# Optimization experiments

Measured on AMD Instinct MI355X. Metric: run time of the kernel, lower is better.

## Reference

```python
import jax, jax.numpy as jnp
import numpy as np

N_GENES = 3072
N_CELLS = 3072
HIDDEN = 64
CAUSAL = 16
CS = 32
ALPHA = 0.35  # LeakyReLU negative slope
NEG_BIG = -9.0e15


def setup_inputs() -> dict:
    key = jax.random.key(0)
    ks = jax.random.split(key, 20)
    s = 0.05
    return {
        "x": jax.random.normal(ks[0], (N_CELLS, N_GENES), jnp.float32),
        "adj": jax.random.randint(ks[1], (N_GENES, N_GENES), 0, 2, jnp.int32),
        "eps": jax.random.normal(ks[2], (N_GENES, CAUSAL), jnp.float32),
        "W_gat": jax.random.normal(ks[3], (N_CELLS, HIDDEN), jnp.float32) * s,
        "a_gat": jax.random.normal(ks[4], (2 * HIDDEN,), jnp.float32) * s,
        "W_mu": jax.random.normal(ks[5], (HIDDEN, CAUSAL), jnp.float32) * s,
        "b_mu": jnp.zeros((CAUSAL,), jnp.float32),
        "W_lv": jax.random.normal(ks[6], (HIDDEN, CAUSAL), jnp.float32) * s,
        "b_lv": jnp.zeros((CAUSAL,), jnp.float32),
        "W_diff": jax.random.normal(ks[7], (CAUSAL + HIDDEN, CS), jnp.float32) * s,
        "b_diff": jnp.zeros((CS,), jnp.float32),
        "W_dec": jax.random.normal(ks[8], (CS, N_CELLS), jnp.float32) * s,
        "b_dec": jnp.zeros((N_CELLS,), jnp.float32),
        "W_gcn1": jax.random.normal(ks[9], (N_CELLS, HIDDEN), jnp.float32) * s,
        "W_gcn2": jax.random.normal(ks[10], (HIDDEN, HIDDEN), jnp.float32) * s,
    }


def _gcn(xg, adjf, W):
    # adj + I, symmetric normalization D^-1/2 A D^-1/2, then A_norm @ (x @ W), relu
    A = adjf + jnp.eye(adjf.shape[0], dtype=adjf.dtype)
    d = A.sum(axis=1)
    d_inv_sqrt = jnp.where(d > 0, d ** -0.5, 0.0)
    A_norm = d_inv_sqrt[:, None] * A * d_inv_sqrt[None, :]
    return jax.nn.relu(A_norm @ (xg @ W))


def reference(x, adj, eps, W_gat, a_gat, W_mu, b_mu, W_lv, b_lv,
              W_diff, b_diff, W_dec, b_dec, W_gcn1, W_gcn2):
    adjf = adj.astype(jnp.float32)
    # ---- GAT layer (batch of 1, squeezed). h: (M, F)
    h = x.T @ W_gat
    F = h.shape[1]
    # a_input[i, j] = concat(h_j, h_i)  => e_ij = leakyrelu(a1.h_j + a2.h_i)
    s_dst = h @ a_gat[:F]   # contribution of column index j
    s_src = h @ a_gat[F:]   # contribution of row index i
    e = jax.nn.leaky_relu(s_src[:, None] + s_dst[None, :], ALPHA)
    e = jnp.where(adjf > 0, e, NEG_BIG)
    att = jax.nn.softmax(e, axis=1)  # dropout p=0.1 is identity in eval mode
    h_gat = jax.nn.elu(att @ h)      # (M, HIDDEN)
    # ---- causal VAE encode + reparameterize
    mu = h_gat @ W_mu + b_mu
    logvar = h_gat @ W_lv + b_lv
    z = mu + eps * jnp.exp(0.5 * logvar)
    # ---- diffusion fusion
    cs = jax.nn.relu(jnp.concatenate([z, h_gat], axis=-1) @ W_diff + b_diff)
    # ---- decoder
    x_recon = jax.nn.sigmoid(cs @ W_dec + b_dec)  # (M, N_CELLS)
    # ---- inference model (two GCN layers on x_recon.T, as in original code)
    h1 = _gcn(x_recon.T, adjf, W_gcn1)
    h2 = _gcn(h1, adjf, W_gcn2)
    ie = jnp.concatenate([h2, cs], axis=-1)
    return (x_recon, h2, ie, cs, mu, logvar)
```

## Files before the change

kernel.cpp:

```cpp
#include <hip/hip_runtime.h>
#include <math.h>

#define N 3072
#define H 64
#define CAUS 16
#define CSD 32
#define GAT_ALPHA 0.35f
#define SLICES 16
#define JSL (N / SLICES)
#define NH (N * H)
typedef unsigned long long u64;
typedef unsigned short u16;
typedef __attribute__((ext_vector_type(4))) float f32x4;
typedef __attribute__((ext_vector_type(8))) short s16x8;
struct alignas(8) u16x4 { u16 x, y, z, w; };
struct T4 { float4 r[4]; };

__device__ inline u16 f2bf(float f) {
  unsigned u = __builtin_bit_cast(unsigned, f);
  u += 0x7fffu + ((u >> 16) & 1u);
  return (u16)(u >> 16);
}

__device__ inline T4 t_load(const float* __restrict__ src, int ld, int t) {
  int k4 = (t >> 4) * 4, m4 = (t & 15) * 4;
  T4 o;
#pragma unroll
  for (int d = 0; d < 4; d++)
    o.r[d] = *(const float4*)(src + (size_t)(k4 + d) * ld + m4);
  return o;
}
__device__ inline void t_store(u16 (&dst)[64][72], const T4& v, int t) {
  int k4 = (t >> 4) * 4, m4 = (t & 15) * 4;
  u16x4 c0 = {f2bf(v.r[0].x), f2bf(v.r[1].x), f2bf(v.r[2].x), f2bf(v.r[3].x)};
  u16x4 c1 = {f2bf(v.r[0].y), f2bf(v.r[1].y), f2bf(v.r[2].y), f2bf(v.r[3].y)};
  u16x4 c2 = {f2bf(v.r[0].z), f2bf(v.r[1].z), f2bf(v.r[2].z), f2bf(v.r[3].z)};
  u16x4 c3 = {f2bf(v.r[0].w), f2bf(v.r[1].w), f2bf(v.r[2].w), f2bf(v.r[3].w)};
  *(u16x4*)&dst[m4 + 0][k4] = c0;
  *(u16x4*)&dst[m4 + 1][k4] = c1;
  *(u16x4*)&dst[m4 + 2][k4] = c2;
  *(u16x4*)&dst[m4 + 3][k4] = c3;
}

__global__ __launch_bounds__(256) void k_pack(const int* __restrict__ adj,
                                              u64* __restrict__ packed,
                                              float* __restrict__ dis) {
  int row = blockIdx.x * 4 + (threadIdx.x >> 6);
  int lane = threadIdx.x & 63;
  const int* ar = adj + (size_t)row * N;
  int deg = 0;
  for (int w = 0; w < 48; w++) {
    int v = ar[w * 64 + lane];
    u64 m = __ballot(v > 0);
    if (lane == 0) packed[(size_t)row * 48 + w] = m;
    deg += (v > 0) ? 1 : 0;
  }
  for (int off = 32; off; off >>= 1) deg += __shfl_xor(deg, off);
  if (lane == 0) dis[row] = rsqrtf((float)deg + 1.0f);
}

__global__ __launch_bounds__(256) void k_mm32(const float* __restrict__ A, int lda,
                                              const float* __restrict__ B, int ldb,
                                              float* __restrict__ outp) {
  __shared__ u16 As[32][72];
  __shared__ u16 Bs[64][72];
  int t = threadIdx.x;
  int g0 = blockIdx.x * 32;
  int c0 = blockIdx.y * JSL;
  int w = t >> 6, l = t & 63, il = l & 15, kg = l >> 4;
  int ri = w & 1, cj = w >> 1;
  int ak = (t >> 3) * 2, am = (t & 7) * 4;
  f32x4 acc0 = {0.f, 0.f, 0.f, 0.f}, acc1 = {0.f, 0.f, 0.f, 0.f};
  float4 a0 = *(const float4*)(A + (size_t)(c0 + ak) * lda + g0 + am);
  float4 a1 = *(const float4*)(A + (size_t)(c0 + ak + 1) * lda + g0 + am);
  T4 bv = t_load(B + (size_t)c0 * ldb, ldb, t);
  for (int cb = 0; cb < JSL; cb += 64) {
    __syncthreads();
    As[am + 0][ak] = f2bf(a0.x); As[am + 1][ak] = f2bf(a0.y);
    As[am + 2][ak] = f2bf(a0.z); As[am + 3][ak] = f2bf(a0.w);
    As[am + 0][ak + 1] = f2bf(a1.x); As[am + 1][ak + 1] = f2bf(a1.y);
    As[am + 2][ak + 1] = f2bf(a1.z); As[am + 3][ak + 1] = f2bf(a1.w);
    t_store(Bs, bv, t);
    if (cb + 64 < JSL) {
      a0 = *(const float4*)(A + (size_t)(c0 + cb + 64 + ak) * lda + g0 + am);
      a1 = *(const float4*)(A + (size_t)(c0 + cb + 65 + ak) * lda + g0 + am);
      bv = t_load(B + (size_t)(c0 + cb + 64) * ldb, ldb, t);
    }
    __syncthreads();
#pragma unroll
    for (int kk = 0; kk < 64; kk += 32) {
      s16x8 a = *(const s16x8*)&As[ri * 16 + il][kk + kg * 8];
      s16x8 b0 = *(const s16x8*)&Bs[cj * 32 + il][kk + kg * 8];
      s16x8 b1 = *(const s16x8*)&Bs[cj * 32 + 16 + il][kk + kg * 8];
      acc0 = __builtin_amdgcn_mfma_f32_16x16x32_bf16(a, b0, acc0, 0, 0, 0);
      acc1 = __builtin_amdgcn_mfma_f32_16x16x32_bf16(a, b1, acc1, 0, 0, 0);
    }
  }
  float* ob = outp + (size_t)blockIdx.y * NH;
#pragma unroll
  for (int c = 0; c < 2; c++) {
    f32x4 acc = c ? acc1 : acc0;
    int col = cj * 32 + c * 16 + il;
    int rbase = g0 + ri * 16 + kg * 4;
#pragma unroll
    for (int r = 0; r < 4; r++)
      ob[(size_t)(rbase + r) * H + col] = acc[r];
  }
}

template <int GAT>
__global__ __launch_bounds__(256) void k_agg(const float* __restrict__ hin,
                                             const u64* __restrict__ packed,
                                             const float* __restrict__ sdst,
                                             const float* __restrict__ ssrc,
                                             const float* __restrict__ dis,
                                             float* __restrict__ outp,
                                             float* __restrict__ zpart) {
  __shared__ u16 Ws[32][72];
  __shared__ u16 Hs[64][72];
  __shared__ float ssl[32];
  int t = threadIdx.x;
  int i0 = blockIdx.x * 32;
  int jbase = blockIdx.y * JSL;
  int w = t >> 6, l = t & 63, il = l & 15, kg = l >> 4;
  int ri = w & 1, cj = w >> 1;
  int r = t >> 3, jq = (t & 7) * 8;
  if (GAT && t < 32) ssl[t] = ssrc[i0 + t];
  __syncthreads();
  float sv = GAT ? ssl[r] : 0.f;
  float zacc = 0.f;
  f32x4 acc0 = {0.f, 0.f, 0.f, 0.f}, acc1 = {0.f, 0.f, 0.f, 0.f};

  auto gen_w = [&](int j0, float (&wv)[8]) {
    u64 wb = packed[(size_t)(i0 + r) * 48 + (j0 >> 6)];
    if (GAT) {
      const float4* s4p = (const float4*)(sdst + j0 + jq);
      float4 s0 = s4p[0], s1 = s4p[1];
      float sf[8] = {s0.x, s0.y, s0.z, s0.w, s1.x, s1.y, s1.z, s1.w};
#pragma unroll
      for (int q = 0; q < 8; q++) {
        float e = sv + sf[q];
        e = e > 0.f ? e : GAT_ALPHA * e;
        float ww = ((wb >> (jq + q)) & 1ULL) ? __expf(e) : 0.f;
        wv[q] = ww;
        zacc += ww;
      }
    } else {
      const float4* d4p = (const float4*)(dis + j0 + jq);
      float4 d0 = d4p[0], d1 = d4p[1];
      float df[8] = {d0.x, d0.y, d0.z, d0.w, d1.x, d1.y, d1.z, d1.w};
#pragma unroll
      for (int q = 0; q < 8; q++) {
        float cnt = (float)((wb >> (jq + q)) & 1ULL) +
                    ((i0 + r) == (j0 + jq + q) ? 1.f : 0.f);
        wv[q] = cnt * df[q];
      }
    }
  };

  T4 hv = t_load(hin + (size_t)jbase * H, H, t);
  float wv[8];
  gen_w(jbase, wv);
  for (int jb = 0; jb < JSL; jb += 64) {
    __syncthreads();
    t_store(Hs, hv, t);
    u16x4 w0 = {f2bf(wv[0]), f2bf(wv[1]), f2bf(wv[2]), f2bf(wv[3])};
    u16x4 w1 = {f2bf(wv[4]), f2bf(wv[5]), f2bf(wv[6]), f2bf(wv[7])};
    *(u16x4*)&Ws[r][jq] = w0;
    *(u16x4*)&Ws[r][jq + 4] = w1;
    if (jb + 64 < JSL) {
      hv = t_load(hin + (size_t)(jbase + jb + 64) * H, H, t);
      gen_w(jbase + jb + 64, wv);
    }
    __syncthreads();
#pragma unroll
    for (int kk = 0; kk < 64; kk += 32) {
      s16x8 a = *(const s16x8*)&Ws[ri * 16 + il][kk + kg * 8];
      s16x8 b0 = *(const s16x8*)&Hs[cj * 32 + il][kk + kg * 8];
      s16x8 b1 = *(const s16x8*)&Hs[cj * 32 + 16 + il][kk + kg * 8];
      acc0 = __builtin_amdgcn_mfma_f32_16x16x32_bf16(a, b0, acc0, 0, 0, 0);
      acc1 = __builtin_amdgcn_mfma_f32_16x16x32_bf16(a, b1, acc1, 0, 0, 0);
    }
  }
  if (GAT) {
    zacc += __shfl_xor(zacc, 1);
    zacc += __shfl_xor(zacc, 2);
    zacc += __shfl_xor(zacc, 4);
    if ((t & 7) == 0) zpart[(size_t)blockIdx.y * N + i0 + r] = zacc;
  }
  float* ob = outp + (size_t)blockIdx.y * NH;
#pragma unroll
  for (int c = 0; c < 2; c++) {
    f32x4 acc = c ? acc1 : acc0;
    int col = cj * 32 + c * 16 + il;
    int rbase = i0 + ri * 16 + kg * 4;
#pragma unroll
    for (int rr = 0; rr < 4; rr++)
      ob[(size_t)(rbase + rr) * H + col] = acc[rr];
  }
}

__global__ __launch_bounds__(256) void k_mmdec32(const float* __restrict__ cs,
                                                 const float* __restrict__ Wdec,
                                                 const float* __restrict__ bdec,
                                                 const float* __restrict__ Wg1,
                                                 float* __restrict__ xr,
                                                 float* __restrict__ outp) {
  __shared__ u16 As[32][72];
  __shared__ u16 Bs[64][72];
  __shared__ u16 Wd[32][40];
  __shared__ u16 Csh[64][40];
  __shared__ float bs_s[32];
  int t = threadIdx.x;
  int g0 = blockIdx.x * 32;
  int c0 = blockIdx.y * JSL;
  int w = t >> 6, l = t & 63, il = l & 15, kg = l >> 4;
  int ri = w & 1, cj = w >> 1;
  {
    int q = t >> 3, m4 = (t & 7) * 4;
    float4 v = *(const float4*)(Wdec + (size_t)q * N + g0 + m4);
    Wd[m4 + 0][q] = f2bf(v.x); Wd[m4 + 1][q] = f2bf(v.y);
    Wd[m4 + 2][q] = f2bf(v.z); Wd[m4 + 3][q] = f2bf(v.w);
    if (t < 32) bs_s[t] = bdec[g0 + t];
  }
  int cell = t >> 3, qf = (t & 7) * 4;
  float4 cv0 = *(const float4*)(cs + (size_t)(c0 + cell) * CSD + qf);
  float4 cv1 = *(const float4*)(cs + (size_t)(c0 + 32 + cell) * CSD + qf);
  T4 bv = t_load(Wg1 + (size_t)c0 * H, H, t);
  f32x4 z = {0.f, 0.f, 0.f, 0.f};
  f32x4 acc0 = z, acc1 = z;
  for (int cb = 0; cb < JSL; cb += 64) {
    __syncthreads();
    u16x4 u0 = {f2bf(cv0.x), f2bf(cv0.y), f2bf(cv0.z), f2bf(cv0.w)};
    u16x4 u1 = {f2bf(cv1.x), f2bf(cv1.y), f2bf(cv1.z), f2bf(cv1.w)};
    *(u16x4*)&Csh[cell][qf] = u0;
    *(u16x4*)&Csh[cell + 32][qf] = u1;
    t_store(Bs, bv, t);
    if (cb + 64 < JSL) {
      cv0 = *(const float4*)(cs + (size_t)(c0 + cb + 64 + cell) * CSD + qf);
      cv1 = *(const float4*)(cs + (size_t)(c0 + cb + 96 + cell) * CSD + qf);
      bv = t_load(Wg1 + (size_t)(c0 + cb + 64) * H, H, t);
    }
    __syncthreads();
    f32x4 dec0 = z, dec1 = z;
    {
      s16x8 a = *(const s16x8*)&Wd[ri * 16 + il][kg * 8];
      s16x8 b0 = *(const s16x8*)&Csh[cj * 32 + il][kg * 8];
      s16x8 b1 = *(const s16x8*)&Csh[cj * 32 + 16 + il][kg * 8];
      dec0 = __builtin_amdgcn_mfma_f32_16x16x32_bf16(a, b0, dec0, 0, 0, 0);
      dec1 = __builtin_amdgcn_mfma_f32_16x16x32_bf16(a, b1, dec1, 0, 0, 0);
    }
#pragma unroll
    for (int c = 0; c < 2; c++) {
      f32x4 dv = c ? dec1 : dec0;
      int kcol = cj * 32 + c * 16 + il;
      int mb = ri * 16 + kg * 4;
      float4 sv4;
      float* sp = (float*)&sv4;
#pragma unroll
      for (int r = 0; r < 4; r++) {
        float pre = dv[r] + bs_s[mb + r];
        float sg = 1.f / (1.f + __expf(-pre));
        sp[r] = sg;
        As[mb + r][kcol] = f2bf(sg);
      }
      *(float4*)(xr + (size_t)(c0 + cb + kcol) * N + g0 + mb) = sv4;
    }
    __syncthreads();
#pragma unroll
    for (int kk = 0; kk < 64; kk += 32) {
      s16x8 a = *(const s16x8*)&As[ri * 16 + il][kk + kg * 8];
      s16x8 b0 = *(const s16x8*)&Bs[cj * 32 + il][kk + kg * 8];
      s16x8 b1 = *(const s16x8*)&Bs[cj * 32 + 16 + il][kk + kg * 8];
      acc0 = __builtin_amdgcn_mfma_f32_16x16x32_bf16(a, b0, acc0, 0, 0, 0);
      acc1 = __builtin_amdgcn_mfma_f32_16x16x32_bf16(a, b1, acc1, 0, 0, 0);
    }
  }
  float* ob = outp + (size_t)blockIdx.y * NH;
#pragma unroll
  for (int c = 0; c < 2; c++) {
    f32x4 acc = c ? acc1 : acc0;
    int col = cj * 32 + c * 16 + il;
    int rbase = g0 + ri * 16 + kg * 4;
#pragma unroll
    for (int r = 0; r < 4; r++)
      ob[(size_t)(rbase + r) * H + col] = acc[r];
  }
}

__global__ __launch_bounds__(256) void k_reduce_sd(const float* __restrict__ src,
                                                   const float* __restrict__ a,
                                                   float* __restrict__ h,
                                                   float* __restrict__ sdst,
                                                   float* __restrict__ ssrc) {
  int row = blockIdx.x * 4 + (threadIdx.x >> 6);
  int lane = threadIdx.x & 63;
  size_t off = (size_t)row * H + lane;
  float v = 0.f;
#pragma unroll
  for (int p = 0; p < SLICES; p++) v += src[(size_t)p * NH + off];
  h[off] = v;
  float d1 = v * a[lane];
  float d2 = v * a[H + lane];
  for (int o = 32; o; o >>= 1) {
    d1 += __shfl_xor(d1, o);
    d2 += __shfl_xor(d2, o);
  }
  if (lane == 0) { sdst[row] = d1; ssrc[row] = d2; }
}

__global__ __launch_bounds__(256) void k_reduce(const float4* __restrict__ src,
                                                float4* __restrict__ dst) {
  int idx = blockIdx.x * 256 + threadIdx.x;
  float4 v = {0, 0, 0, 0};
#pragma unroll
  for (int p = 0; p < SLICES; p++) {
    float4 u = src[(size_t)p * (NH / 4) + idx];
    v.x += u.x; v.y += u.y; v.z += u.z; v.w += u.w;
  }
  dst[idx] = v;
}

__global__ __launch_bounds__(256) void k_vae(const float* __restrict__ hacc,
                                             const float* __restrict__ zpart,
                                             const float* __restrict__ eps,
                                             const float* __restrict__ Wmu,
                                             const float* __restrict__ bmu,
                                             const float* __restrict__ Wlv,
                                             const float* __restrict__ blv,
                                             const float* __restrict__ Wd,
                                             const float* __restrict__ bd,
                                             float* __restrict__ mu_o,
                                             float* __restrict__ lv_o,
                                             float* __restrict__ cs_o,
                                             float* __restrict__ ie) {
  __shared__ float hs[16][65];
  __shared__ float zs[16][17];
  __shared__ float wmu_s[1024];
  __shared__ float wlv_s[1024];
  __shared__ float wd_s[2560];
  int t = threadIdx.x;
  int row0 = blockIdx.x * 16;
  {
    int rr = t >> 4, pp = t & 15;
    float zv = zpart[(size_t)pp * N + row0 + rr];
    zv += __shfl_xor(zv, 1);
    zv += __shfl_xor(zv, 2);
    zv += __shfl_xor(zv, 4);
    zv += __shfl_xor(zv, 8);
    float zi = 1.0f / fmaxf(zv, 1e-30f);
    const float4* g4 = (const float4*)(hacc + (size_t)row0 * H);
    float4 v = {0, 0, 0, 0};
#pragma unroll
    for (int p = 0; p < SLICES; p++) {
      float4 u = g4[(size_t)p * (NH / 4) + t];
      v.x += u.x; v.y += u.y; v.z += u.z; v.w += u.w;
    }
    int c0 = (t & 15) * 4;
    float e0 = v.x * zi, e1 = v.y * zi, e2 = v.z * zi, e3 = v.w * zi;
    hs[rr][c0 + 0] = e0 > 0.f ? e0 : __expf(e0) - 1.f;
    hs[rr][c0 + 1] = e1 > 0.f ? e1 : __expf(e1) - 1.f;
    hs[rr][c0 + 2] = e2 > 0.f ? e2 : __expf(e2) - 1.f;
    hs[rr][c0 + 3] = e3 > 0.f ? e3 : __expf(e3) - 1.f;
  }
#pragma unroll
  for (int k = 0; k < 4; k++) {
    int lin = t + k * 256;
    wmu_s[lin] = Wmu[lin];
    wlv_s[lin] = Wlv[lin];
  }
#pragma unroll
  for (int k = 0; k < 10; k++) {
    int lin = t + k * 256;
    wd_s[lin] = Wd[lin];
  }
  __syncthreads();
  int r = t >> 4, kk = t & 15;
  float mu = bmu[kk], lv = blv[kk];
#pragma unroll 8
  for (int l = 0; l < 64; l++) {
    float hv = hs[r][l];
    mu += hv * wmu_s[l * 16 + kk];
    lv += hv * wlv_s[l * 16 + kk];
  }
  float zc = mu + eps[(size_t)(row0 + r) * CAUS + kk] * __expf(0.5f * lv);
  mu_o[(size_t)(row0 + r) * CAUS + kk] = mu;
  lv_o[(size_t)(row0 + r) * CAUS + kk] = lv;
  zs[r][kk] = zc;
  __syncthreads();
#pragma unroll
  for (int p = 0; p < 2; p++) {
    int lin = t + p * 256;
    int rr = lin >> 5, c = lin & 31;
    float acc = bd[c];
#pragma unroll 4
    for (int q = 0; q < 16; q++) acc += zs[rr][q] * wd_s[q * 32 + c];
#pragma unroll 8
    for (int l = 0; l < 64; l++) acc += hs[rr][l] * wd_s[(16 + l) * 32 + c];
    float v = fmaxf(acc, 0.f);
    cs_o[(size_t)(row0 + rr) * CSD + c] = v;
    ie[(size_t)(row0 + rr) * 96 + 64 + c] = v;
  }
}

__global__ __launch_bounds__(256) void k_h1w2(const float* __restrict__ h1src,
                                              const float* __restrict__ dis,
                                              const float* __restrict__ W2,
                                              float* __restrict__ t2) {
  __shared__ float w2s[64 * 64];
  __shared__ float hs[4][65];
  int t = threadIdx.x;
  int row0 = blockIdx.x * 4;
#pragma unroll
  for (int k = 0; k < 16; k++) w2s[t + k * 256] = W2[t + k * 256];
  {
    int rr = t >> 6;
    size_t off = (size_t)row0 * H + t;
    float v = 0.f;
#pragma unroll
    for (int p = 0; p < SLICES; p++) v += h1src[(size_t)p * NH + off];
    hs[rr][t & 63] = fmaxf(v * dis[row0 + rr], 0.f);
  }
  __syncthreads();
  int r = t >> 6, f = t & 63;
  float acc = 0.f;
#pragma unroll 8
  for (int l = 0; l < 64; l++) acc += hs[r][l] * w2s[l * 64 + f];
  t2[(size_t)(row0 + r) * H + f] = acc;
}

__global__ __launch_bounds__(256) void k_fin2(const float* __restrict__ h2src,
                                              const float* __restrict__ dis,
                                              float* __restrict__ h2,
                                              float* __restrict__ ie) {
  int idx = blockIdx.x * 256 + threadIdx.x;
  int row = idx >> 6, f = idx & 63;
  float v = 0.f;
#pragma unroll
  for (int p = 0; p < SLICES; p++) v += h2src[(size_t)p * NH + idx];
  v = fmaxf(v * dis[row], 0.f);
  h2[idx] = v;
  ie[(size_t)row * 96 + f] = v;
}

extern "C" void kernel_launch(void* const* d_in, const int* in_sizes, int n_in,
                              void* d_out, int out_size, void* d_ws, size_t ws_size,
                              hipStream_t stream) {
  const float* x    = (const float*)d_in[0];
  const int*   adj  = (const int*)d_in[1];
  const float* eps  = (const float*)d_in[2];
  const float* Wgat = (const float*)d_in[3];
  const float* agat = (const float*)d_in[4];
  const float* Wmu  = (const float*)d_in[5];
  const float* bmu  = (const float*)d_in[6];
  const float* Wlv  = (const float*)d_in[7];
  const float* blv  = (const float*)d_in[8];
  const float* Wdif = (const float*)d_in[9];
  const float* bdif = (const float*)d_in[10];
  const float* Wdec = (const float*)d_in[11];
  const float* bdec = (const float*)d_in[12];
  const float* Wg1  = (const float*)d_in[13];
  const float* Wg2  = (const float*)d_in[14];

  float* out = (float*)d_out;
  float* xr  = out;
  float* h2  = out + 9437184;
  float* ie  = out + 9633792;
  float* cs  = out + 9928704;
  float* muo = out + 10027008;
  float* lvo = out + 10076160;

  u64* packed = (u64*)d_ws;
  float* wf    = (float*)d_ws + 294912;
  float* part  = wf;
  float* h     = part + (size_t)SLICES * NH;
  float* t1    = h + NH;
  float* t2    = t1 + NH;
  float* sdst  = t2 + NH;
  float* ssrc  = sdst + N;
  float* dis   = ssrc + N;
  float* zpart = dis + N;

  k_mm32<<<dim3(96, SLICES), 256, 0, stream>>>(x, N, Wgat, H, part);
  k_pack<<<768, 256, 0, stream>>>(adj, packed, dis);
  k_reduce_sd<<<768, 256, 0, stream>>>(part, agat, h, sdst, ssrc);
  k_agg<1><<<dim3(96, SLICES), 256, 0, stream>>>(h, packed, sdst, ssrc, dis,
                                                 part, zpart);
  k_vae<<<192, 256, 0, stream>>>(part, zpart, eps, Wmu, bmu, Wlv, blv,
                                 Wdif, bdif, muo, lvo, cs, ie);
  k_mmdec32<<<dim3(96, SLICES), 256, 0, stream>>>(cs, Wdec, bdec, Wg1, xr, part);
  k_reduce<<<192, 256, 0, stream>>>((const float4*)part, (float4*)t1);
  k_agg<0><<<dim3(96, SLICES), 256, 0, stream>>>(t1, packed, nullptr, nullptr,
                                                 dis, part, nullptr);
  k_h1w2<<<768, 256, 0, stream>>>(part, dis, Wg2, t2);
  k_agg<0><<<dim3(96, SLICES), 256, 0, stream>>>(t2, packed, nullptr, nullptr,
                                                 dis, part, nullptr);
  k_fin2<<<768, 256, 0, stream>>>(part, dis, h2, ie);
}
```

Before: 118.1 us.

## Fuse adjacency packing into first GEMM launch and halve split-K slices

```diff
diff --git a/kernel.cpp b/kernel.cpp
--- a/kernel.cpp
+++ b/kernel.cpp
@@ -6,7 +6,7 @@
 #define CAUS 16
 #define CSD 32
 #define GAT_ALPHA 0.35f
-#define SLICES 16
+#define SLICES 8
 #define JSL (N / SLICES)
 #define NH (N * H)
 typedef unsigned long long u64;
@@ -42,38 +42,41 @@
   *(u16x4*)&dst[m4 + 3][k4] = c3;
 }
 
-__global__ __launch_bounds__(256) void k_pack(const int* __restrict__ adj,
+__global__ __launch_bounds__(256) void k_mmpk(const float* __restrict__ A,
+                                              const float* __restrict__ B,
+                                              float* __restrict__ outp,
+                                              const int* __restrict__ adj,
                                               u64* __restrict__ packed,
                                               float* __restrict__ dis) {
-  int row = blockIdx.x * 4 + (threadIdx.x >> 6);
-  int lane = threadIdx.x & 63;
-  const int* ar = adj + (size_t)row * N;
-  int deg = 0;
-  for (int w = 0; w < 48; w++) {
-    int v = ar[w * 64 + lane];
-    u64 m = __ballot(v > 0);
-    if (lane == 0) packed[(size_t)row * 48 + w] = m;
-    deg += (v > 0) ? 1 : 0;
-  }
-  for (int off = 32; off; off >>= 1) deg += __shfl_xor(deg, off);
-  if (lane == 0) dis[row] = rsqrtf((float)deg + 1.0f);
-}
-
-__global__ __launch_bounds__(256) void k_mm32(const float* __restrict__ A, int lda,
-                                              const float* __restrict__ B, int ldb,
-                                              float* __restrict__ outp) {
   __shared__ u16 As[32][72];
   __shared__ u16 Bs[64][72];
+  int bid = blockIdx.x;
   int t = threadIdx.x;
-  int g0 = blockIdx.x * 32;
-  int c0 = blockIdx.y * JSL;
+  if (bid >= 768) {
+    int row = (bid - 768) * 4 + (t >> 6);
+    int lane = t & 63;
+    const int* ar = adj + (size_t)row * N;
+    int deg = 0;
+    for (int w = 0; w < 48; w++) {
+      int v = ar[w * 64 + lane];
+      u64 m = __ballot(v > 0);
+      if (lane == 0) packed[(size_t)row * 48 + w] = m;
+      deg += (v > 0) ? 1 : 0;
+    }
+    for (int off = 32; off; off >>= 1) deg += __shfl_xor(deg, off);
+    if (lane == 0) dis[row] = rsqrtf((float)deg + 1.0f);
+    return;
+  }
+  int g0 = (bid % 96) * 32;
+  int sl = bid / 96;
+  int c0 = sl * JSL;
   int w = t >> 6, l = t & 63, il = l & 15, kg = l >> 4;
   int ri = w & 1, cj = w >> 1;
   int ak = (t >> 3) * 2, am = (t & 7) * 4;
   f32x4 acc0 = {0.f, 0.f, 0.f, 0.f}, acc1 = {0.f, 0.f, 0.f, 0.f};
-  float4 a0 = *(const float4*)(A + (size_t)(c0 + ak) * lda + g0 + am);
-  float4 a1 = *(const float4*)(A + (size_t)(c0 + ak + 1) * lda + g0 + am);
-  T4 bv = t_load(B + (size_t)c0 * ldb, ldb, t);
+  float4 a0 = *(const float4*)(A + (size_t)(c0 + ak) * N + g0 + am);
+  float4 a1 = *(const float4*)(A + (size_t)(c0 + ak + 1) * N + g0 + am);
+  T4 bv = t_load(B + (size_t)c0 * H, H, t);
   for (int cb = 0; cb < JSL; cb += 64) {
     __syncthreads();
     As[am + 0][ak] = f2bf(a0.x); As[am + 1][ak] = f2bf(a0.y);
@@ -82,9 +85,9 @@
     As[am + 2][ak + 1] = f2bf(a1.z); As[am + 3][ak + 1] = f2bf(a1.w);
     t_store(Bs, bv, t);
     if (cb + 64 < JSL) {
-      a0 = *(const float4*)(A + (size_t)(c0 + cb + 64 + ak) * lda + g0 + am);
-      a1 = *(const float4*)(A + (size_t)(c0 + cb + 65 + ak) * lda + g0 + am);
-      bv = t_load(B + (size_t)(c0 + cb + 64) * ldb, ldb, t);
+      a0 = *(const float4*)(A + (size_t)(c0 + cb + 64 + ak) * N + g0 + am);
+      a1 = *(const float4*)(A + (size_t)(c0 + cb + 65 + ak) * N + g0 + am);
+      bv = t_load(B + (size_t)(c0 + cb + 64) * H, H, t);
     }
     __syncthreads();
 #pragma unroll
@@ -96,7 +99,7 @@
       acc1 = __builtin_amdgcn_mfma_f32_16x16x32_bf16(a, b1, acc1, 0, 0, 0);
     }
   }
-  float* ob = outp + (size_t)blockIdx.y * NH;
+  float* ob = outp + (size_t)sl * NH;
 #pragma unroll
   for (int c = 0; c < 2; c++) {
     f32x4 acc = c ? acc1 : acc0;
@@ -343,7 +346,7 @@
   int row0 = blockIdx.x * 16;
   {
     int rr = t >> 4, pp = t & 15;
-    float zv = zpart[(size_t)pp * N + row0 + rr];
+    float zv = (pp < SLICES) ? zpart[(size_t)pp * N + row0 + rr] : 0.f;
     zv += __shfl_xor(zv, 1);
     zv += __shfl_xor(zv, 2);
     zv += __shfl_xor(zv, 4);
@@ -481,8 +484,7 @@
   float* dis   = ssrc + N;
   float* zpart = dis + N;
 
-  k_mm32<<<dim3(96, SLICES), 256, 0, stream>>>(x, N, Wgat, H, part);
-  k_pack<<<768, 256, 0, stream>>>(adj, packed, dis);
+  k_mmpk<<<1536, 256, 0, stream>>>(x, Wgat, part, adj, packed, dis);
   k_reduce_sd<<<768, 256, 0, stream>>>(part, agat, h, sdst, ssrc);
   k_agg<1><<<dim3(96, SLICES), 256, 0, stream>>>(h, packed, sdst, ssrc, dis,
                                                  part, zpart);
```

New measurement: 100.9 us. 1.17x faster.
